# Performance work log

Hardware: AMD Instinct MI355X
Metric: run time of the kernel (lower is better)

## Reference

```python
import jax, jax.numpy as jnp
import numpy as np

N = 512       # nodes
V = 8         # n_vectors_hidden
F = 128       # n_invariant_feat_hidden
H = 8         # num_heads
BESSEL = 8
R_MAX = 10.0
FH = F // H
VH = V // H

def _edges(n):
    s, r = np.meshgrid(np.arange(n), np.arange(n), indexing='ij')
    m = s != r
    return jnp.asarray(s[m], jnp.int32), jnp.asarray(r[m], jnp.int32)

def _sph(v):
    # real spherical harmonics ell=1,2,3, e3nn 'component' normalization, unit input v[...,3] -> [...,15]
    x, y, z = v[..., 0], v[..., 1], v[..., 2]
    s3, s15, s5 = np.sqrt(3.0), np.sqrt(15.0), np.sqrt(5.0)
    sh1 = jnp.stack([x, y, z], -1) * s3
    sh2 = jnp.stack([s15 * x * y, s15 * y * z, 0.5 * s5 * (3 * z**2 - 1), s15 * x * z, 0.5 * s15 * (x**2 - y**2)], -1)
    c33, c32, c31, c30 = np.sqrt(35.0 / 8.0), np.sqrt(105.0), np.sqrt(21.0 / 8.0), 0.5 * np.sqrt(7.0)
    sh3 = jnp.stack([c33 * y * (3 * x**2 - y**2), c32 * x * y * z, c31 * y * (5 * z**2 - 1), c30 * z * (5 * z**2 - 3), c31 * x * (5 * z**2 - 1), 0.5 * c32 * z * (x**2 - y**2), c33 * x * (x**2 - 3 * y**2)], -1)
    return jnp.concatenate([sh1, sh2, sh3], -1)

def _bessel(x, n, x_max):
    # e3nn.bessel basis: sqrt(2/x_max) * sin(k*pi*x/x_max) / x, k=1..n
    x = x[..., None]
    k = jnp.arange(1, n + 1, dtype=x.dtype)
    x_safe = jnp.where(x == 0, 1.0, x)
    return np.sqrt(2.0 / x_max) * jnp.sin(k * jnp.pi * x / x_max) / x_safe

def _sus(x):
    return jnp.where(x > 0, jnp.exp(-1.0 / jnp.where(x > 0, x, 1.0)), 0.0)

def _soft_envelope(x, x_max, a=2.0, v0=1.2):
    return v0 * _sus(a * (1.0 - x / x_max)) / _sus(jnp.asarray(a, x.dtype))

def _forward(positions, features, We0, be0, We1, be1, Wq, Wk, Wek, Wv, Wev, Wg, Wo0, bo0, Wo1, bo1, Wo2, bo2):
    n = positions.shape[0]
    senders, receivers = _edges(n)
    vec = positions[senders] - positions[receivers]               # [E,V,3] gather
    lengths = jnp.sqrt(jnp.sum(vec * vec, -1) + 1e-20)            # safe_norm [E,V]
    unit = vec / lengths[..., None]
    sph = _sph(unit)                                              # [E,V,15]
    radial = _bessel(lengths, BESSEL, R_MAX) * _soft_envelope(lengths, R_MAX)[..., None]  # [E,V,B]
    e_scal = radial.reshape(radial.shape[0], -1)                  # [E, V*B]
    h = jax.nn.silu(e_scal @ We0 + be0)
    h = jax.nn.silu(h @ We1 + be1)                                # edge MLP, output_activation=silu
    E = h.shape[0]
    q = (features @ Wq).reshape(n, H, FH)
    k = (features[senders] @ Wk + h @ Wek).reshape(E, H, FH)
    logits = jnp.einsum('ehf,ehf->eh', q[receivers], k) / np.sqrt(FH)
    seg_max = jax.ops.segment_max(logits, receivers, num_segments=n)
    ex = jnp.exp(logits - seg_max[receivers])                     # edge_weight_cutoff = 1
    denom = jax.ops.segment_sum(ex, receivers, num_segments=n)
    alpha = ex / denom[receivers]                                 # [E,H] per-receiver softmax
    v_s = (features[senders] @ Wv + h @ Wev).reshape(E, H, FH)
    gate = h @ Wg                                                 # [E,V] invariant gates
    v_vec = (gate[..., None] * sph[..., :3]).reshape(E, H, VH, 3) # equivariant values from ell=1 sph
    agg_s = jax.ops.segment_sum(alpha[..., None] * v_s, receivers, num_segments=n).reshape(n, F)
    agg_v = jax.ops.segment_sum(alpha[:, :, None, None] * v_vec, receivers, num_segments=n).reshape(n, V, 3)
    o = jax.nn.silu(agg_s @ Wo0 + bo0)
    o = jax.nn.silu(o @ Wo1 + bo1)
    o = o @ Wo2 + bo2                                             # hk MLP: last layer linear
    return (positions + agg_v, features + o)

def setup_inputs() -> dict:
    key = jax.random.key(0)
    ks = jax.random.split(key, 16)
    def w(k, i, o):
        return jax.random.normal(k, (i, o), jnp.float32) / np.sqrt(i)
    M = 128
    D = V * BESSEL
    return {
        'positions': jax.random.normal(ks[0], (N, V, 3), jnp.float32),
        'features': jax.random.normal(ks[1], (N, F), jnp.float32),
        'We0': w(ks[2], D, M), 'be0': jnp.zeros((M,), jnp.float32),
        'We1': w(ks[3], M, M), 'be1': jnp.zeros((M,), jnp.float32),
        'Wq': w(ks[4], F, F), 'Wk': w(ks[5], F, F), 'Wek': w(ks[6], M, F),
        'Wv': w(ks[7], F, F), 'Wev': w(ks[8], M, F), 'Wg': w(ks[9], M, V),
        'Wo0': w(ks[10], F, M), 'bo0': jnp.zeros((M,), jnp.float32),
        'Wo1': w(ks[11], M, M), 'bo1': jnp.zeros((M,), jnp.float32),
        'Wo2': w(ks[12], M, F), 'bo2': jnp.zeros((F,), jnp.float32),
    }

def reference(positions, features, We0, be0, We1, be1, Wq, Wk, Wek, Wv, Wev, Wg, Wo0, bo0, Wo1, bo1, Wo2, bo2):
    return _forward(positions, features, We0, be0, We1, be1, Wq, Wk, Wek, Wv, Wev, Wg, Wo0, bo0, Wo1, bo1, Wo2, bo2)
```

## Files before the change

### kernel.cpp

```cpp
#include <hip/hip_runtime.h>
#include <hip/hip_bf16.h>

#define WS_KNB  0
#define WS_VNT  32768
#define WS_AW2  65536
#define WS_W0T  1114112
#define WS_W1T  1118208
#define WS_PS   1126400
#define PS_STRIDE 1072

typedef short bf16x8 __attribute__((ext_vector_type(8)));
typedef short short4v __attribute__((ext_vector_type(4)));
typedef float f32x4 __attribute__((ext_vector_type(4)));
typedef unsigned short ushort_t;

static __device__ __forceinline__ ushort_t f2b(float x) {
  __hip_bfloat16 h = __float2bfloat16(x);
  return reinterpret_cast<ushort_t&>(h);
}
static __device__ __forceinline__ float b2f(ushort_t u) {
  unsigned v = ((unsigned)u) << 16;
  return reinterpret_cast<float&>(v);
}
static __device__ __forceinline__ float fsilu(float x) {
  return x * __builtin_amdgcn_rcpf(1.f + __expf(-x));
}

static __device__ __forceinline__ bf16x8 radial_frag(
    float dx, float dy, float dz, float& ux, float& uy, float& uz)
{
  const float l2 = fmaf(dx,dx, fmaf(dy,dy, fmaf(dz,dz, 1e-20f)));
  const float inv = rsqrtf(l2);
  const float len = l2 * inv;
  ux = dx*inv; uy = dy*inv; uz = dz*inv;
  const float yy = 2.f - len*0.2f;
  const float env = (yy > 0.f) ? 1.9784655648f * __expf(-__builtin_amdgcn_rcpf(yy)) : 0.f;
  const float coef = 0.4472135955f * env * inv;
  const float arg = len * 0.31415926535f;
  const float s1v = __sinf(arg), c1v = __cosf(arg);
  const float twc = 2.f*c1v;
  float sp = 0.f, sc = s1v;
  bf16x8 ev;
#pragma unroll
  for (int bb = 0; bb < 8; ++bb) {
    ev[bb] = (short)f2b(coef*sc);
    const float nx = fmaf(twc, sc, -sp);
    sp = sc; sc = nx;
  }
  return ev;
}

__global__ __launch_bounds__(128) void k_prep(
    const float* __restrict__ feat, const float* __restrict__ Wq,
    const float* __restrict__ Wk, const float* __restrict__ Wv,
    const float* __restrict__ Wek, const float* __restrict__ Wg,
    const float* __restrict__ We0, const float* __restrict__ We1,
    float* __restrict__ ws)
{
  const int blk = blockIdx.x, j = threadIdx.x;
  if (blk >= 512) {
    const int i = (blk - 512)*128 + j;
    ushort_t* W0T = (ushort_t*)(ws + WS_W0T);
    ushort_t* W1T = (ushort_t*)(ws + WS_W1T);
    if (i < 8192) {
      const int n = i >> 6, k = i & 63;
      W0T[n*64 + k] = f2b(We0[k*128 + n]);
    } else {
      const int t = i - 8192, n = t >> 7, k = t & 127;
      W1T[n*128 + k] = f2b(We1[k*128 + n]);
    }
    return;
  }
  const int r = blk;
  __shared__ float fr[128];
  __shared__ float qL[128];
  fr[j] = feat[r*128 + j];
  __syncthreads();
  float aq = 0.f, ak = 0.f, av = 0.f;
#pragma unroll 4
  for (int i = 0; i < 128; ++i) {
    const float f = fr[i];
    aq = fmaf(f, Wq[i*128 + j], aq);
    ak = fmaf(f, Wk[i*128 + j], ak);
    av = fmaf(f, Wv[i*128 + j], av);
  }
  ushort_t* knB = (ushort_t*)(ws + WS_KNB);
  ushort_t* vnT = (ushort_t*)(ws + WS_VNT);
  knB[r*128 + j] = f2b(ak);
  vnT[j*512 + r] = f2b(av);
  qL[j] = aq;
  __syncthreads();
  ushort_t* AW = (ushort_t*)(ws + WS_AW2) + r*4096;
  const float* wr = Wek + j*128;
  const int jh = j >> 4;
#pragma unroll
  for (int h = 0; h < 8; ++h) {
    float acc = 0.f;
#pragma unroll
    for (int f = 0; f < 16; ++f)
      acc = fmaf(wr[16*h + f], qL[16*h + f], acc);
    AW[h*256 + j] = f2b(acc * 0.25f);
    AW[h*256 + 128 + j] = (h == jh) ? f2b(0.25f * aq) : (ushort_t)0;
  }
#pragma unroll
  for (int v = 0; v < 8; ++v) {
    AW[(8 + v)*256 + j] = f2b(Wg[j*8 + v]);
    AW[(8 + v)*256 + 128 + j] = 0;
  }
}

#define MFMA(a,b,c) __builtin_amdgcn_mfma_f32_16x16x32_bf16((a),(b),(c),0,0,0)

__global__ __launch_bounds__(512) void k_edge10(
    const float* __restrict__ pos,
    const float* __restrict__ be0, const float* __restrict__ be1,
    float* __restrict__ ws)
{
  __shared__ __align__(16) char Lds[51360];
  ushort_t* Es   = (ushort_t*)(Lds);
  ushort_t* H1   = (ushort_t*)(Lds + 8192);
  ushort_t* H2t  = (ushort_t*)(Lds + 24576);
  float*    lgT0 = (float*)(Lds + 40960);
  float*    lgT1 = (float*)(Lds + 45120);
  ushort_t* Pb   = (ushort_t*)(Lds + 49280);
  float*    rscL = (float*)(Lds + 51328);

  const int tid = threadIdx.x;
  const int nw = tid >> 6, l = tid & 63;
  const int c = l & 15, g = l >> 4;
  const int b = blockIdx.x;
  const int r = b >> 1, half = b & 1;
  const int base = half * 256;

  const ushort_t* knB = (const ushort_t*)(ws + WS_KNB);
  const ushort_t* vnT = (const ushort_t*)(ws + WS_VNT);
  const ushort_t* AW2 = (const ushort_t*)(ws + WS_AW2) + r*4096;
  const ushort_t* W0T = (const ushort_t*)(ws + WS_W0T);
  const ushort_t* W1T = (const ushort_t*)(ws + WS_W1T);

  const int ncol = nw*16 + c;
  const float be0v = be0[ncol], be1v = be1[ncol];
  const bf16x8 w0f0 = *(const bf16x8*)(W0T + ncol*64 + g*8);
  const bf16x8 w0f1 = *(const bf16x8*)(W0T + ncol*64 + 32 + g*8);
  const int m_lg = nw & 3, kh = nw >> 2;

  const float prx = pos[r*24 + nw*3 + 0];
  const float pry = pos[r*24 + nw*3 + 1];
  const float prz = pos[r*24 + nw*3 + 2];

  f32x4 bh = {0,0,0,0}, sna = {0,0,0,0};
  float avx = 0.f, avy = 0.f, avz = 0.f;
  float mrun = -1e30f, drun = 0.f;
  float ux, uy, uz;

  {
    const int sg = base + l;
    const bf16x8 ev = radial_frag(pos[sg*24 + nw*3 + 0] - prx,
                                  pos[sg*24 + nw*3 + 1] - pry,
                                  pos[sg*24 + nw*3 + 2] - prz, ux, uy, uz);
    *(bf16x8*)(Es + l*64 + ((nw ^ (l&7))<<3)) = ev;
  }
  __syncthreads();

  for (int tile = 0; tile < 4; ++tile) {
    const int gbase = base + tile*64;

    float npx = 0.f, npy = 0.f, npz = 0.f;
    if (tile < 3) {
      const int sg = gbase + 64 + l;
      npx = pos[sg*24 + nw*3 + 0];
      npy = pos[sg*24 + nw*3 + 1];
      npz = pos[sg*24 + nw*3 + 2];
    }

#pragma unroll
    for (int m = 0; m < 4; ++m) {
      const int ra = m*16 + c;
      const bf16x8 e0 = *(const bf16x8*)(Es + ra*64 + (((g  ) ^ (ra&7))<<3));
      const bf16x8 e1 = *(const bf16x8*)(Es + ra*64 + (((4+g) ^ (ra&7))<<3));
      f32x4 acc = {0,0,0,0};
      acc = MFMA(e0, w0f0, acc);
      acc = MFMA(e1, w0f1, acc);
#pragma unroll
      for (int i = 0; i < 4; ++i) {
        const int row = m*16 + g*4 + i;
        H1[row*128 + (((ncol>>3) ^ (row&15))<<3) + (c&7)] =
            f2b(fsilu(acc[i] + be0v));
      }
    }
    __syncthreads();

    f32x4 a1[4];
#pragma unroll
    for (int m = 0; m < 4; ++m) {
      const int ra = m*16 + c;
      f32x4 acc = {0,0,0,0};
#pragma unroll
      for (int kb = 0; kb < 4; ++kb) {
        const bf16x8 af = *(const bf16x8*)(H1 + ra*128 + (((kb*4+g) ^ (ra&15))<<3));
        const bf16x8 wf = *(const bf16x8*)(W1T + ncol*128 + kb*32 + g*8);
        acc = MFMA(af, wf, acc);
      }
      a1[m] = acc;
    }
    float nux = 0.f, nuy = 0.f, nuz = 0.f;
    if (tile < 3) {
      const bf16x8 ev = radial_frag(npx - prx, npy - pry, npz - prz, nux, nuy, nuz);
      *(bf16x8*)(Es + l*64 + ((nw ^ (l&7))<<3)) = ev;
    }
    __syncthreads();

    bf16x8 knf[4];
    if (kh == 1) {
#pragma unroll
      for (int kb = 0; kb < 4; ++kb)
        knf[kb] = *(const bf16x8*)(knB + (gbase + m_lg*16 + c)*128 + kb*32 + g*8);
    }
#pragma unroll
    for (int m = 0; m < 4; ++m) {
      short4v pk;
#pragma unroll
      for (int i = 0; i < 4; ++i) {
        const int row = m*16 + g*4 + i;
        const ushort_t bv = f2b(fsilu(a1[m][i] + be1v));
        H1[row*128 + (((ncol>>3) ^ (row&15))<<3) + (c&7)] = bv;
        pk[i] = (short)bv;
      }
      *(short4v*)(H2t + ncol*64 + (((m*2 + (g>>1)) ^ (ncol&7))<<3) + ((g&1)<<2)) = pk;
    }
    __syncthreads();

    {
      const int ra = m_lg*16 + c;
      f32x4 lg = {0,0,0,0};
      if (kh == 0) {
#pragma unroll
        for (int kb = 0; kb < 4; ++kb) {
          const bf16x8 af = *(const bf16x8*)(H1 + ra*128 + (((kb*4+g) ^ (ra&15))<<3));
          const bf16x8 aw = *(const bf16x8*)(AW2 + c*256 + kb*32 + g*8);
          lg = MFMA(af, aw, lg);
        }
      } else {
#pragma unroll
        for (int kb = 0; kb < 4; ++kb) {
          const bf16x8 aw = *(const bf16x8*)(AW2 + c*256 + 128 + kb*32 + g*8);
          lg = MFMA(knf[kb], aw, lg);
        }
      }
      float* lgW = kh ? lgT1 : lgT0;
#pragma unroll
      for (int i = 0; i < 4; ++i)
        lgW[c*65 + m_lg*16 + g*4 + i] = lg[i];
    }
    __syncthreads();

    const bf16x8 vnf0 = *(const bf16x8*)(vnT + ncol*512 + gbase + g*8);
    const bf16x8 vnf1 = *(const bf16x8*)(vnT + ncol*512 + gbase + 32 + g*8);
    {
      const int h = nw;
      float lgv = lgT0[h*65 + l] + lgT1[h*65 + l];
      const float gate = lgT0[(8+h)*65 + l] + lgT1[(8+h)*65 + l];
      if (gbase + l == r) lgv = -1e30f;
      float t = lgv;
      t = fmaxf(t, __shfl_xor(t, 1));
      t = fmaxf(t, __shfl_xor(t, 2));
      t = fmaxf(t, __shfl_xor(t, 4));
      t = fmaxf(t, __shfl_xor(t, 8));
      t = fmaxf(t, __shfl_xor(t, 16));
      t = fmaxf(t, __shfl_xor(t, 32));
      const float mnew = fmaxf(mrun, t);
      const float rsc = __expf(mrun - mnew);
      mrun = mnew;
      const float val = __expf(lgv - mnew);
      float wsm = val;
      wsm += __shfl_xor(wsm, 1);
      wsm += __shfl_xor(wsm, 2);
      wsm += __shfl_xor(wsm, 4);
      wsm += __shfl_xor(wsm, 8);
      wsm += __shfl_xor(wsm, 16);
      wsm += __shfl_xor(wsm, 32);
      drun = drun*rsc + wsm;
      const float ga = val * gate;
      Pb[h*64 + (((l>>3) ^ h)<<3) + (l&7)] = f2b(val);
      Pb[(8+h)*64 + (((l>>3) ^ h)<<3) + (l&7)] = f2b(ga);
      if (l == 0) rscL[h] = rsc;
      avx = avx*rsc + ga*ux;
      avy = avy*rsc + ga*uy;
      avz = avz*rsc + ga*uz;
    }
    __syncthreads();

    {
      float rs[4];
#pragma unroll
      for (int i = 0; i < 4; ++i) rs[i] = rscL[(4*g + i) & 7];
#pragma unroll
      for (int i = 0; i < 4; ++i) { bh[i] *= rs[i]; sna[i] *= rs[i]; }
      const bf16x8 pa0 = *(const bf16x8*)(Pb + c*64 + (((g  ) ^ (c&7))<<3));
      const bf16x8 pa1 = *(const bf16x8*)(Pb + c*64 + (((4+g) ^ (c&7))<<3));
      bh = MFMA(pa0, *(const bf16x8*)(H2t + ncol*64 + (((g  ) ^ (ncol&7))<<3)), bh);
      bh = MFMA(pa1, *(const bf16x8*)(H2t + ncol*64 + (((4+g) ^ (ncol&7))<<3)), bh);
      sna = MFMA(pa0, vnf0, sna);
      sna = MFMA(pa1, vnf1, sna);
    }
    if (tile < 3) { ux = nux; uy = nuy; uz = nuz; }
  }

  float* PSf = ws + WS_PS + b*PS_STRIDE;
  ushort_t* PSs = (ushort_t*)PSf;
  if (g < 2) {
#pragma unroll
    for (int i = 0; i < 4; ++i) {
      PSs[(4*g + i)*128 + ncol] = f2b(bh[i]);
      PSs[1024 + (4*g + i)*128 + ncol] = f2b(sna[i]);
    }
  }
  avx += __shfl_xor(avx, 1); avy += __shfl_xor(avy, 1); avz += __shfl_xor(avz, 1);
  avx += __shfl_xor(avx, 2); avy += __shfl_xor(avy, 2); avz += __shfl_xor(avz, 2);
  avx += __shfl_xor(avx, 4); avy += __shfl_xor(avy, 4); avz += __shfl_xor(avz, 4);
  avx += __shfl_xor(avx, 8); avy += __shfl_xor(avy, 8); avz += __shfl_xor(avz, 8);
  avx += __shfl_xor(avx,16); avy += __shfl_xor(avy,16); avz += __shfl_xor(avz,16);
  avx += __shfl_xor(avx,32); avy += __shfl_xor(avy,32); avz += __shfl_xor(avz,32);
  if (l == 0) {
    PSf[1024 + nw*3 + 0] = avx;
    PSf[1024 + nw*3 + 1] = avy;
    PSf[1024 + nw*3 + 2] = avz;
    PSf[1048 + nw] = mrun;
    PSf[1056 + nw] = drun;
  }
}

__global__ __launch_bounds__(128) void k_merge(
    const float* __restrict__ pos, const float* __restrict__ feat,
    const float* __restrict__ Wev,
    const float* __restrict__ Wo0, const float* __restrict__ bo0,
    const float* __restrict__ Wo1, const float* __restrict__ bo1,
    const float* __restrict__ Wo2, const float* __restrict__ bo2,
    const float* __restrict__ ws, float* __restrict__ out)
{
  const int r = blockIdx.x, j = threadIdx.x;
  __shared__ float S1s[8], S2s[8], Dh[8];
  __shared__ float BhC[1024];
  __shared__ float asB[128], o1[128], o2[128];
  const float* P1f = ws + WS_PS + (2*r)*PS_STRIDE;
  const float* P2f = P1f + PS_STRIDE;
  const ushort_t* P1s = (const ushort_t*)P1f;
  const ushort_t* P2s = (const ushort_t*)P2f;
  if (j < 8) {
    const float m1 = P1f[1048 + j], m2 = P2f[1048 + j];
    const float M = fmaxf(m1, m2);
    const float s1 = __expf(m1 - M), s2 = __expf(m2 - M);
    S1s[j] = s1; S2s[j] = s2;
    Dh[j] = s1*P1f[1056 + j] + s2*P2f[1056 + j];
  }
  __syncthreads();
#pragma unroll
  for (int h = 0; h < 8; ++h)
    BhC[h*128 + j] = S1s[h]*b2f(P1s[h*128 + j]) + S2s[h]*b2f(P2s[h*128 + j]);
  const int hh = j >> 4;
  const float snj = S1s[hh]*b2f(P1s[1024 + hh*128 + j])
                  + S2s[hh]*b2f(P2s[1024 + hh*128 + j]);
  if (j < 24) {
    const int v = j / 3;
    const float avc = S1s[v]*P1f[1024 + j] + S2s[v]*P2f[1024 + j];
    out[r*24 + j] = pos[r*24 + j]
        + 1.7320508076f * avc * __builtin_amdgcn_rcpf(Dh[v]);
  }
  __syncthreads();
  {
    float ev = 0.f;
#pragma unroll 4
    for (int m = 0; m < 128; ++m)
      ev = fmaf(BhC[hh*128 + m], Wev[m*128 + j], ev);
    asB[j] = (snj + ev) * __builtin_amdgcn_rcpf(Dh[hh]);
  }
  __syncthreads();
  {
    float acc = bo0[j];
#pragma unroll 4
    for (int i = 0; i < 128; ++i) acc = fmaf(asB[i], Wo0[i*128 + j], acc);
    o1[j] = fsilu(acc);
  }
  __syncthreads();
  {
    float acc = bo1[j];
#pragma unroll 4
    for (int i = 0; i < 128; ++i) acc = fmaf(o1[i], Wo1[i*128 + j], acc);
    o2[j] = fsilu(acc);
  }
  __syncthreads();
  {
    float acc = bo2[j];
#pragma unroll 4
    for (int i = 0; i < 128; ++i) acc = fmaf(o2[i], Wo2[i*128 + j], acc);
    out[12288 + r*128 + j] = feat[r*128 + j] + acc;
  }
}

extern "C" void kernel_launch(void* const* d_in, const int* in_sizes, int n_in,
                              void* d_out, int out_size, void* d_ws, size_t ws_size,
                              hipStream_t stream)
{
  const float* pos  = (const float*)d_in[0];
  const float* feat = (const float*)d_in[1];
  const float* We0  = (const float*)d_in[2];
  const float* be0  = (const float*)d_in[3];
  const float* We1  = (const float*)d_in[4];
  const float* be1  = (const float*)d_in[5];
  const float* Wq   = (const float*)d_in[6];
  const float* Wk   = (const float*)d_in[7];
  const float* Wek  = (const float*)d_in[8];
  const float* Wv   = (const float*)d_in[9];
  const float* Wev  = (const float*)d_in[10];
  const float* Wg   = (const float*)d_in[11];
  const float* Wo0  = (const float*)d_in[12];
  const float* bo0  = (const float*)d_in[13];
  const float* Wo1  = (const float*)d_in[14];
  const float* bo1  = (const float*)d_in[15];
  const float* Wo2  = (const float*)d_in[16];
  const float* bo2  = (const float*)d_in[17];
  float* ws  = (float*)d_ws;
  float* out = (float*)d_out;

  hipLaunchKernelGGL(k_prep, dim3(704), dim3(128), 0, stream,
                     feat, Wq, Wk, Wv, Wek, Wg, We0, We1, ws);
  hipLaunchKernelGGL(k_edge10, dim3(1024), dim3(512), 0, stream,
                     pos, be0, be1, ws);
  hipLaunchKernelGGL(k_merge, dim3(512), dim3(128), 0, stream,
                     pos, feat, Wev, Wo0, bo0, Wo1, bo1, Wo2, bo2, ws, out);
}
```

Before: 113.8 us.

## Shrink edge kernel LDS and registers to raise occupancy via buffer aliasing

Cuts the edge kernel's shared memory from about 51KB to 40KB by aliasing H1 with Pb/rscL and Es with the logit tables. The second-layer activations are no longer written back to H1. The logit MFMA is transposed to read H2t directly, and the logit tables use an XOR swizzle in place of padding. Register pressure drops because W0 fragments, knB fragments and vn fragments are loaded right before use, and the next tile's radial basis is computed at the end of the loop behind an extra barrier. A launch bound of 4 is added so two 512-thread blocks can share a CU, at the cost of an extra sync per tile, strided 2-byte LDS gathers, and less latency hiding for the global loads.

```diff
diff --git a/kernel.cpp b/kernel.cpp
--- a/kernel.cpp
+++ b/kernel.cpp
@@ -111,19 +111,19 @@
 
 #define MFMA(a,b,c) __builtin_amdgcn_mfma_f32_16x16x32_bf16((a),(b),(c),0,0,0)
 
-__global__ __launch_bounds__(512) void k_edge10(
+__global__ __launch_bounds__(512, 4) void k_edge11(
     const float* __restrict__ pos,
     const float* __restrict__ be0, const float* __restrict__ be1,
     float* __restrict__ ws)
 {
-  __shared__ __align__(16) char Lds[51360];
-  ushort_t* Es   = (ushort_t*)(Lds);
-  ushort_t* H1   = (ushort_t*)(Lds + 8192);
-  ushort_t* H2t  = (ushort_t*)(Lds + 24576);
-  float*    lgT0 = (float*)(Lds + 40960);
-  float*    lgT1 = (float*)(Lds + 45120);
-  ushort_t* Pb   = (ushort_t*)(Lds + 49280);
-  float*    rscL = (float*)(Lds + 51328);
+  __shared__ __align__(16) char Lds[40960];
+  ushort_t* H1   = (ushort_t*)(Lds);
+  ushort_t* Pb   = (ushort_t*)(Lds);
+  float*    rscL = (float*)(Lds + 2048);
+  ushort_t* H2t  = (ushort_t*)(Lds + 16384);
+  ushort_t* Es   = (ushort_t*)(Lds + 32768);
+  float*    lgT0 = (float*)(Lds + 32768);
+  float*    lgT1 = (float*)(Lds + 36864);
 
   const int tid = threadIdx.x;
   const int nw = tid >> 6, l = tid & 63;
@@ -140,8 +140,6 @@
 
   const int ncol = nw*16 + c;
   const float be0v = be0[ncol], be1v = be1[ncol];
-  const bf16x8 w0f0 = *(const bf16x8*)(W0T + ncol*64 + g*8);
-  const bf16x8 w0f1 = *(const bf16x8*)(W0T + ncol*64 + 32 + g*8);
   const int m_lg = nw & 3, kh = nw >> 2;
 
   const float prx = pos[r*24 + nw*3 + 0];
@@ -173,24 +171,27 @@
       npz = pos[sg*24 + nw*3 + 2];
     }
 
-#pragma unroll
-    for (int m = 0; m < 4; ++m) {
-      const int ra = m*16 + c;
-      const bf16x8 e0 = *(const bf16x8*)(Es + ra*64 + (((g  ) ^ (ra&7))<<3));
-      const bf16x8 e1 = *(const bf16x8*)(Es + ra*64 + (((4+g) ^ (ra&7))<<3));
-      f32x4 acc = {0,0,0,0};
-      acc = MFMA(e0, w0f0, acc);
-      acc = MFMA(e1, w0f1, acc);
-#pragma unroll
-      for (int i = 0; i < 4; ++i) {
-        const int row = m*16 + g*4 + i;
-        H1[row*128 + (((ncol>>3) ^ (row&15))<<3) + (c&7)] =
-            f2b(fsilu(acc[i] + be0v));
+    {
+      const bf16x8 w0f0 = *(const bf16x8*)(W0T + ncol*64 + g*8);
+      const bf16x8 w0f1 = *(const bf16x8*)(W0T + ncol*64 + 32 + g*8);
+#pragma unroll
+      for (int m = 0; m < 4; ++m) {
+        const int ra = m*16 + c;
+        const bf16x8 e0 = *(const bf16x8*)(Es + ra*64 + (((g  ) ^ (ra&7))<<3));
+        const bf16x8 e1 = *(const bf16x8*)(Es + ra*64 + (((4+g) ^ (ra&7))<<3));
+        f32x4 acc = {0,0,0,0};
+        acc = MFMA(e0, w0f0, acc);
+        acc = MFMA(e1, w0f1, acc);
+#pragma unroll
+        for (int i = 0; i < 4; ++i) {
+          const int row = m*16 + g*4 + i;
+          H1[row*128 + (((ncol>>3) ^ (row&15))<<3) + (c&7)] =
+              f2b(fsilu(acc[i] + be0v));
+        }
       }
     }
     __syncthreads();
 
-    f32x4 a1[4];
 #pragma unroll
     for (int m = 0; m < 4; ++m) {
       const int ra = m*16 + c;
@@ -201,65 +202,52 @@
         const bf16x8 wf = *(const bf16x8*)(W1T + ncol*128 + kb*32 + g*8);
         acc = MFMA(af, wf, acc);
       }
-      a1[m] = acc;
-    }
-    float nux = 0.f, nuy = 0.f, nuz = 0.f;
-    if (tile < 3) {
-      const bf16x8 ev = radial_frag(npx - prx, npy - pry, npz - prz, nux, nuy, nuz);
-      *(bf16x8*)(Es + l*64 + ((nw ^ (l&7))<<3)) = ev;
+      short4v pk;
+#pragma unroll
+      for (int i = 0; i < 4; ++i)
+        pk[i] = (short)f2b(fsilu(acc[i] + be1v));
+      *(short4v*)(H2t + ncol*64 + (((m*2 + (g>>1)) ^ (ncol&7))<<3) + (g&1)*4) = pk;
     }
     __syncthreads();
 
-    bf16x8 knf[4];
-    if (kh == 1) {
-#pragma unroll
-      for (int kb = 0; kb < 4; ++kb)
-        knf[kb] = *(const bf16x8*)(knB + (gbase + m_lg*16 + c)*128 + kb*32 + g*8);
-    }
-#pragma unroll
-    for (int m = 0; m < 4; ++m) {
-      short4v pk;
-#pragma unroll
-      for (int i = 0; i < 4; ++i) {
-        const int row = m*16 + g*4 + i;
-        const ushort_t bv = f2b(fsilu(a1[m][i] + be1v));
-        H1[row*128 + (((ncol>>3) ^ (row&15))<<3) + (c&7)] = bv;
-        pk[i] = (short)bv;
-      }
-      *(short4v*)(H2t + ncol*64 + (((m*2 + (g>>1)) ^ (ncol&7))<<3) + ((g&1)<<2)) = pk;
-    }
-    __syncthreads();
-
     {
-      const int ra = m_lg*16 + c;
       f32x4 lg = {0,0,0,0};
       if (kh == 0) {
+        const int rb = m_lg*2 + (c>>3);
+        const int rl = c & 7;
 #pragma unroll
         for (int kb = 0; kb < 4; ++kb) {
-          const bf16x8 af = *(const bf16x8*)(H1 + ra*128 + (((kb*4+g) ^ (ra&15))<<3));
+          bf16x8 bb;
+#pragma unroll
+          for (int j = 0; j < 8; ++j)
+            bb[j] = (short)H2t[(kb*32 + g*8 + j)*64 + ((rb ^ j)<<3) + rl];
           const bf16x8 aw = *(const bf16x8*)(AW2 + c*256 + kb*32 + g*8);
-          lg = MFMA(af, aw, lg);
+          lg = MFMA(aw, bb, lg);
         }
       } else {
+        const int srow = gbase + m_lg*16 + c;
 #pragma unroll
         for (int kb = 0; kb < 4; ++kb) {
+          const bf16x8 bb = *(const bf16x8*)(knB + srow*128 + kb*32 + g*8);
           const bf16x8 aw = *(const bf16x8*)(AW2 + c*256 + 128 + kb*32 + g*8);
-          lg = MFMA(knf[kb], aw, lg);
+          lg = MFMA(aw, bb, lg);
         }
       }
       float* lgW = kh ? lgT1 : lgT0;
 #pragma unroll
-      for (int i = 0; i < 4; ++i)
-        lgW[c*65 + m_lg*16 + g*4 + i] = lg[i];
+      for (int i = 0; i < 4; ++i) {
+        const int ch = g*4 + i;
+        lgW[ch*64 + ((m_lg*16 + c) ^ (g<<4))] = lg[i];
+      }
     }
     __syncthreads();
 
-    const bf16x8 vnf0 = *(const bf16x8*)(vnT + ncol*512 + gbase + g*8);
-    const bf16x8 vnf1 = *(const bf16x8*)(vnT + ncol*512 + gbase + 32 + g*8);
     {
       const int h = nw;
-      float lgv = lgT0[h*65 + l] + lgT1[h*65 + l];
-      const float gate = lgT0[(8+h)*65 + l] + lgT1[(8+h)*65 + l];
+      const int kv = (h>>2)<<4;
+      const int kg = ((8+h)>>2)<<4;
+      float lgv = lgT0[h*64 + (l ^ kv)] + lgT1[h*64 + (l ^ kv)];
+      const float gate = lgT0[(8+h)*64 + (l ^ kg)] + lgT1[(8+h)*64 + (l ^ kg)];
       if (gbase + l == r) lgv = -1e30f;
       float t = lgv;
       t = fmaxf(t, __shfl_xor(t, 1));
@@ -300,10 +288,16 @@
       const bf16x8 pa1 = *(const bf16x8*)(Pb + c*64 + (((4+g) ^ (c&7))<<3));
       bh = MFMA(pa0, *(const bf16x8*)(H2t + ncol*64 + (((g  ) ^ (ncol&7))<<3)), bh);
       bh = MFMA(pa1, *(const bf16x8*)(H2t + ncol*64 + (((4+g) ^ (ncol&7))<<3)), bh);
+      const bf16x8 vnf0 = *(const bf16x8*)(vnT + ncol*512 + gbase + g*8);
+      const bf16x8 vnf1 = *(const bf16x8*)(vnT + ncol*512 + gbase + 32 + g*8);
       sna = MFMA(pa0, vnf0, sna);
       sna = MFMA(pa1, vnf1, sna);
     }
-    if (tile < 3) { ux = nux; uy = nuy; uz = nuz; }
+    if (tile < 3) {
+      const bf16x8 ev = radial_frag(npx - prx, npy - pry, npz - prz, ux, uy, uz);
+      *(bf16x8*)(Es + l*64 + ((nw ^ (l&7))<<3)) = ev;
+      __syncthreads();
+    }
   }
 
   float* PSf = ws + WS_PS + b*PS_STRIDE;
@@ -424,7 +418,7 @@
 
   hipLaunchKernelGGL(k_prep, dim3(704), dim3(128), 0, stream,
                      feat, Wq, Wk, Wv, Wek, Wg, We0, We1, ws);
-  hipLaunchKernelGGL(k_edge10, dim3(1024), dim3(512), 0, stream,
+  hipLaunchKernelGGL(k_edge11, dim3(1024), dim3(512), 0, stream,
                      pos, be0, be1, ws);
   hipLaunchKernelGGL(k_merge, dim3(512), dim3(128), 0, stream,
                      pos, feat, Wev, Wo0, bo0, Wo1, bo1, Wo2, bo2, ws, out);
```

New measurement: 103.1 us. -9.4%, faster.
